# Kernel tuning notes

Measured on AMD Instinct MI355X. Metric: run time of the kernel, lower is better.

## Reference

```python
import jax, jax.numpy as jnp
import numpy as np

B, T, D = 4, 4096, 1024
H, HD = 16, 64
EPS = 1e-6


def setup_inputs() -> dict:
    key = jax.random.key(0)
    ks = jax.random.split(key, 5)
    scale = 1.0 / np.sqrt(D)
    return {
        "x": jax.random.normal(ks[0], (B, T, D), dtype=jnp.float32),
        "Wq": jax.random.normal(ks[1], (D, H * HD), dtype=jnp.float32) * scale,
        "Wk": jax.random.normal(ks[2], (D, H * HD), dtype=jnp.float32) * scale,
        "Wv": jax.random.normal(ks[3], (D, H * HD), dtype=jnp.float32) * scale,
        "Wo": jax.random.normal(ks[4], (H * HD, D), dtype=jnp.float32) * scale,
    }


def _feature_map(x):
    # ELU + 1 feature map (always positive)
    return jax.nn.elu(x) + 1.0


def _causal_linear_attention(q, k, v, eps=EPS):
    # q,k,v: (B,H,T,Dk/Dv) -> scan over T with running state
    Dk = q.shape[-1]
    Dv = v.shape[-1]
    qT = jnp.moveaxis(q, 2, 0)  # (T,B,H,Dk)
    kT = jnp.moveaxis(k, 2, 0)
    vT = jnp.moveaxis(v, 2, 0)

    S0 = jnp.zeros((q.shape[0], q.shape[1], Dk, Dv), dtype=q.dtype)
    z0 = jnp.zeros((q.shape[0], q.shape[1], Dk), dtype=q.dtype)

    def step(carry, qkv_t):
        S, z = carry
        q_t, k_t, v_t = qkv_t
        S = S + jnp.einsum('bhd,bhe->bhde', k_t, v_t)
        z = z + k_t
        num = jnp.einsum('bhd,bhde->bhe', q_t, S)
        den = jnp.einsum('bhd,bhd->bh', q_t, z) + eps
        return (S, z), num / den[..., None]

    _, yT = jax.lax.scan(step, (S0, z0), (qT, kT, vT))  # yT: (T,B,H,Dv)
    return jnp.moveaxis(yT, 0, 2)  # (B,H,T,Dv)


def reference(x, Wq, Wk, Wv, Wo):
    b, t, _ = x.shape

    def proj(W):
        return (x @ W).reshape(b, t, H, HD).transpose(0, 2, 1, 3)  # (B,H,T,HD)

    q = _feature_map(proj(Wq))
    k = _feature_map(proj(Wk))
    v = proj(Wv)
    y = _causal_linear_attention(q, k, v)  # (B,H,T,HD)
    y = y.transpose(0, 2, 1, 3).reshape(b, t, H * HD)
    return y @ Wo
```

## Files before the change

### kernel.cpp

```cpp
#include <hip/hip_runtime.h>


typedef __bf16 bf16;
typedef __bf16 bf16x8 __attribute__((ext_vector_type(8)));
typedef float f32x4 __attribute__((ext_vector_type(4)));

#define EPS 1e-6f

__device__ __forceinline__ void gl_lds16(const void* g, void* l) {
  __builtin_amdgcn_global_load_lds(
      (__attribute__((address_space(1))) void*)g,
      (__attribute__((address_space(3))) void*)l, 16, 0, 0);
}

__device__ __forceinline__ float fmact(float v) {
  return v > 0.f ? v + 1.f : __expf(v);
}

__global__ __launch_bounds__(256) void cvt_bf16(const float* __restrict__ in,
                                                bf16* __restrict__ out, int n8) {
  int i = blockIdx.x * 256 + threadIdx.x;
  if (i >= n8) return;
  size_t base = (size_t)i * 8;
  float4 v0 = *(const float4*)&in[base];
  float4 v1 = *(const float4*)&in[base + 4];
  bf16x8 o;
  o[0] = (bf16)v0.x; o[1] = (bf16)v0.y; o[2] = (bf16)v0.z; o[3] = (bf16)v0.w;
  o[4] = (bf16)v1.x; o[5] = (bf16)v1.y; o[6] = (bf16)v1.z; o[7] = (bf16)v1.w;
  *(bf16x8*)&out[base] = o;
}

__global__ __launch_bounds__(256) void wtrans(const float* __restrict__ W,
                                              bf16* __restrict__ WT) {
  __shared__ float tile[64][65];
  const int k0 = blockIdx.x * 64, n0 = blockIdx.y * 64;
  const int t = threadIdx.x;
  {
    const int r4 = t / 16, c4 = (t % 16) * 4;
#pragma unroll
    for (int rr = 0; rr < 4; ++rr) {
      int r = r4 + rr * 16;
      float4 v = *(const float4*)&W[(size_t)(k0 + r) * 1024 + n0 + c4];
      tile[r][c4] = v.x; tile[r][c4 + 1] = v.y;
      tile[r][c4 + 2] = v.z; tile[r][c4 + 3] = v.w;
    }
  }
  __syncthreads();
  const int nl = t / 4, kb = (t % 4) * 16;
  bf16x8 o0, o1;
#pragma unroll
  for (int j = 0; j < 8; ++j) {
    o0[j] = (bf16)tile[kb + j][nl];
    o1[j] = (bf16)tile[kb + 8 + j][nl];
  }
  *(bf16x8*)&WT[(size_t)(n0 + nl) * 1024 + k0 + kb] = o0;
  *(bf16x8*)&WT[(size_t)(n0 + nl) * 1024 + k0 + kb + 8] = o1;
}

template <int PROJ>
__global__ __launch_bounds__(256) void gemm_bt(const bf16* __restrict__ A,
                                               const bf16* __restrict__ BT,
                                               bf16* __restrict__ Obf,
                                               float* __restrict__ Of, int N) {
  __shared__ alignas(16) bf16 As[128 * 32];
  __shared__ alignas(16) bf16 Bs[128 * 32];
  const int t = threadIdx.x;
  const int m0 = blockIdx.x * 128, n0 = blockIdx.y * 128;
  const int l = t & 63, w = t >> 6;
  const int wm = (w >> 1) * 64, wn = (w & 1) * 64;
  const int lr = l & 15, lg = l >> 4, lk = lg * 8;
  f32x4 acc[4][4] = {};
  const int ar = t >> 2;
  const int ac = (t & 3) * 8;
  bf16* asw = As + w * 512;
  bf16* bsw = Bs + w * 512;
  const bf16* pa0 = A + (size_t)(m0 + ar) * 1024 + ac;
  const bf16* pa1 = A + (size_t)(m0 + ar + 64) * 1024 + ac;
  const bf16* pb0 = BT + (size_t)(n0 + ar) * 1024 + ac;
  const bf16* pb1 = BT + (size_t)(n0 + ar + 64) * 1024 + ac;
  for (int k0 = 0; k0 < 1024; k0 += 32) {
    gl_lds16(pa0 + k0, asw);
    gl_lds16(pa1 + k0, asw + 2048);
    gl_lds16(pb0 + k0, bsw);
    gl_lds16(pb1 + k0, bsw + 2048);
    __syncthreads();
    bf16x8 af[4], bfv[4];
#pragma unroll
    for (int m = 0; m < 4; ++m)
      af[m] = *(const bf16x8*)&As[(wm + m * 16 + lr) * 32 + lk];
#pragma unroll
    for (int n = 0; n < 4; ++n)
      bfv[n] = *(const bf16x8*)&Bs[(wn + n * 16 + lr) * 32 + lk];
#pragma unroll
    for (int m = 0; m < 4; ++m)
#pragma unroll
      for (int n = 0; n < 4; ++n)
        acc[m][n] = __builtin_amdgcn_mfma_f32_16x16x32_bf16(af[m], bfv[n],
                                                            acc[m][n], 0, 0, 0);
    __syncthreads();
  }
  const size_t ldo = (size_t)N;
#pragma unroll
  for (int m = 0; m < 4; ++m)
#pragma unroll
    for (int n = 0; n < 4; ++n)
#pragma unroll
      for (int r = 0; r < 4; ++r) {
        int row = m0 + wm + m * 16 + lg * 4 + r;
        int col = n0 + wn + n * 16 + lr;
        float v = acc[m][n][r];
        if (PROJ) {
          if (col < 2048) v = fmact(v);
          Obf[(size_t)row * ldo + col] = (bf16)v;
        } else {
          Of[(size_t)row * ldo + col] = v;
        }
      }
}

__global__ __launch_bounds__(256) void chunk_ktv(const bf16* __restrict__ QKV,
                                                 float* __restrict__ S_ws,
                                                 float* __restrict__ z_ws) {
  const int blk = blockIdx.x;
  const int bh = blk >> 5, c = blk & 31;
  const int b = bh >> 4, h = bh & 15;
  const size_t rowbase = (size_t)b * 4096 + (size_t)c * 128;
  __shared__ alignas(16) bf16 KT[64 * 136];
  __shared__ alignas(16) bf16 VT[64 * 136];
  const int t = threadIdx.x;
  {
    const int r = t >> 1, c0 = (t & 1) * 32;
    const bf16* kp = QKV + (rowbase + r) * 3072 + 1024 + h * 64 + c0;
    const bf16* vp = QKV + (rowbase + r) * 3072 + 2048 + h * 64 + c0;
    bf16x8 kv[4], vv[4];
#pragma unroll
    for (int q8 = 0; q8 < 4; ++q8) {
      kv[q8] = *(const bf16x8*)&kp[q8 * 8];
      vv[q8] = *(const bf16x8*)&vp[q8 * 8];
    }
#pragma unroll
    for (int q8 = 0; q8 < 4; ++q8)
#pragma unroll
      for (int j = 0; j < 8; ++j) {
        KT[(c0 + q8 * 8 + j) * 136 + r] = kv[q8][j];
        VT[(c0 + q8 * 8 + j) * 136 + r] = vv[q8][j];
      }
  }
  __syncthreads();
  if (t < 64) {
    float z = 0.f;
    for (int tt = 0; tt < 128; ++tt) z += (float)KT[t * 136 + tt];
    z_ws[(size_t)blk * 64 + t] = z;
  }
  const int l = t & 63, w = t >> 6;
  const int lr = l & 15, lg = l >> 4, lk = lg * 8;
  f32x4 acc[4] = {};
#pragma unroll
  for (int ks = 0; ks < 4; ++ks) {
    const int k0 = ks * 32;
    bf16x8 a = *(const bf16x8*)&KT[(w * 16 + lr) * 136 + k0 + lk];
#pragma unroll
    for (int n = 0; n < 4; ++n) {
      bf16x8 bv = *(const bf16x8*)&VT[(n * 16 + lr) * 136 + k0 + lk];
      acc[n] = __builtin_amdgcn_mfma_f32_16x16x32_bf16(a, bv, acc[n], 0, 0, 0);
    }
  }
#pragma unroll
  for (int n = 0; n < 4; ++n)
#pragma unroll
    for (int r = 0; r < 4; ++r) {
      int d = w * 16 + lg * 4 + r;
      int e = n * 16 + lr;
      S_ws[((size_t)blk * 64 + d) * 64 + e] = acc[n][r];
    }
}

__global__ __launch_bounds__(256) void prefix_scan(const float* __restrict__ S_ws,
                                                   const float* __restrict__ z_ws,
                                                   bf16* __restrict__ STp,
                                                   float* __restrict__ zP) {
  const int bh = blockIdx.x;
  const int t = threadIdx.x;
  __shared__ float sbuf[4096];
  float racc[16];
#pragma unroll
  for (int u = 0; u < 16; ++u) racc[u] = 0.f;
  const int e = t >> 2, d0 = (t & 3) * 16;
  float zr = 0.f;
  for (int c = 0; c < 32; ++c) {
    const size_t cb = (size_t)bh * 32 + c;
    bf16x8 o0, o1;
#pragma unroll
    for (int u = 0; u < 8; ++u) {
      o0[u] = (bf16)racc[u];
      o1[u] = (bf16)racc[8 + u];
    }
    *(bf16x8*)&STp[cb * 4096 + e * 64 + d0] = o0;
    *(bf16x8*)&STp[cb * 4096 + e * 64 + d0 + 8] = o1;
    if (t < 64) {
      zP[cb * 64 + t] = zr;
      zr += z_ws[cb * 64 + t];
    }
    const float* Sc = S_ws + cb * 4096;
#pragma unroll
    for (int q4 = 0; q4 < 4; ++q4)
      *(float4*)&sbuf[t * 16 + q4 * 4] = *(const float4*)&Sc[t * 16 + q4 * 4];
    __syncthreads();
#pragma unroll
    for (int u = 0; u < 16; ++u) racc[u] += sbuf[(d0 + u) * 64 + e];
    __syncthreads();
  }
}

__global__ __launch_bounds__(256) void chunk_attn(const bf16* __restrict__ QKV,
                                                  const bf16* __restrict__ STp,
                                                  const float* __restrict__ zP,
                                                  bf16* __restrict__ Y) {
  const int blk = blockIdx.x;
  const int bh = blk >> 5, c = blk & 31;
  const int b = bh >> 4, h = bh & 15;
  const size_t cb = (size_t)bh * 32 + c;
  const size_t rowbase = (size_t)b * 4096 + (size_t)c * 128;
  const bf16* Q = QKV + rowbase * 3072 + h * 64;
  const bf16* K = QKV + rowbase * 3072 + 1024 + h * 64;
  const bf16* V = QKV + rowbase * 3072 + 2048 + h * 64;
  __shared__ alignas(16) bf16 VT[64 * 136];
  __shared__ alignas(16) bf16 P[128 * 136];
  __shared__ float den[128];
  const int t = threadIdx.x;
  {
    const int r = t >> 1, c0 = (t & 1) * 32;
    const bf16* vp = V + (size_t)r * 3072 + c0;
    bf16x8 vv[4];
#pragma unroll
    for (int q8 = 0; q8 < 4; ++q8) vv[q8] = *(const bf16x8*)&vp[q8 * 8];
#pragma unroll
    for (int q8 = 0; q8 < 4; ++q8)
#pragma unroll
      for (int j = 0; j < 8; ++j) VT[(c0 + q8 * 8 + j) * 136 + r] = vv[q8][j];
  }
  const int l = t & 63, w = t >> 6;
  const int lr = l & 15, lg = l >> 4, lk = lg * 8;
  f32x4 acc[2][4] = {};
  f32x4 accs[2][8] = {};
#pragma unroll
  for (int kq = 0; kq < 2; ++kq) {
    const int k0 = kq * 32;
    bf16x8 am[2];
#pragma unroll
    for (int m = 0; m < 2; ++m)
      am[m] = *(const bf16x8*)&Q[(size_t)(w * 32 + m * 16 + lr) * 3072 + k0 + lk];
#pragma unroll
    for (int n = 0; n < 4; ++n) {
      bf16x8 bs = *(const bf16x8*)&STp[cb * 4096 + (size_t)(n * 16 + lr) * 64 + k0 + lk];
#pragma unroll
      for (int m = 0; m < 2; ++m)
        acc[m][n] = __builtin_amdgcn_mfma_f32_16x16x32_bf16(am[m], bs, acc[m][n], 0, 0, 0);
    }
#pragma unroll
    for (int n = 0; n < 8; ++n) {
      bf16x8 bk = *(const bf16x8*)&K[(size_t)(n * 16 + lr) * 3072 + k0 + lk];
#pragma unroll
      for (int m = 0; m < 2; ++m)
        accs[m][n] = __builtin_amdgcn_mfma_f32_16x16x32_bf16(am[m], bk, accs[m][n], 0, 0, 0);
    }
  }
#pragma unroll
  for (int m = 0; m < 2; ++m)
#pragma unroll
    for (int r = 0; r < 4; ++r) {
      const int row_c = w * 32 + m * 16 + lg * 4 + r;
      float s = 0.f;
#pragma unroll
      for (int n = 0; n < 8; ++n) {
        const int col_c = n * 16 + lr;
        float v = accs[m][n][r];
        v = (col_c <= row_c) ? v : 0.f;
        accs[m][n][r] = v;
        s += v;
      }
      s += __shfl_xor(s, 1);
      s += __shfl_xor(s, 2);
      s += __shfl_xor(s, 4);
      s += __shfl_xor(s, 8);
      if (lr == 0) den[row_c] = s;
#pragma unroll
      for (int n = 0; n < 8; ++n)
        P[row_c * 136 + n * 16 + lr] = (bf16)accs[m][n][r];
    }
  __syncthreads();
  if (t < 128) {
    float s = EPS;
    const bf16* qr = Q + (size_t)t * 3072;
    const float* zp = zP + cb * 64;
#pragma unroll
    for (int d8 = 0; d8 < 64; d8 += 8) {
      bf16x8 qv = *(const bf16x8*)&qr[d8];
#pragma unroll
      for (int j = 0; j < 8; ++j) s += (float)qv[j] * zp[d8 + j];
    }
    den[t] += s;
  }
#pragma unroll
  for (int ks = 0; ks < 4; ++ks) {
    const int k0 = ks * 32;
    bf16x8 ap[2];
#pragma unroll
    for (int m = 0; m < 2; ++m)
      ap[m] = *(const bf16x8*)&P[(w * 32 + m * 16 + lr) * 136 + k0 + lk];
#pragma unroll
    for (int n = 0; n < 4; ++n) {
      bf16x8 bv = *(const bf16x8*)&VT[(n * 16 + lr) * 136 + k0 + lk];
#pragma unroll
      for (int m = 0; m < 2; ++m)
        acc[m][n] = __builtin_amdgcn_mfma_f32_16x16x32_bf16(ap[m], bv, acc[m][n], 0, 0, 0);
    }
  }
  __syncthreads();
#pragma unroll
  for (int m = 0; m < 2; ++m)
#pragma unroll
    for (int n = 0; n < 4; ++n)
#pragma unroll
      for (int r = 0; r < 4; ++r) {
        const int row_c = w * 32 + m * 16 + lg * 4 + r;
        const int col = n * 16 + lr;
        float y = acc[m][n][r] / den[row_c];
        Y[(rowbase + row_c) * 1024 + h * 64 + col] = (bf16)y;
      }
}

extern "C" void kernel_launch(void* const* d_in, const int* in_sizes, int n_in,
                              void* d_out, int out_size, void* d_ws, size_t ws_size,
                              hipStream_t stream) {
  (void)in_sizes; (void)n_in; (void)out_size; (void)ws_size;
  const float* x  = (const float*)d_in[0];
  const float* Wq = (const float*)d_in[1];
  const float* Wk = (const float*)d_in[2];
  const float* Wv = (const float*)d_in[3];
  const float* Wo = (const float*)d_in[4];
  char* ws = (char*)d_ws;
  bf16*  XB   = (bf16*)ws;
  bf16*  WT3  = (bf16*)(ws + 33554432);
  bf16*  WOT  = (bf16*)(ws + 39845888);
  bf16*  QKV  = (bf16*)(ws + 41943040);
  float* S_ws = (float*)(ws + 142606336);
  float* z_ws = (float*)(ws + 176160768);
  bf16*  STp  = (bf16*)(ws + 176685056);
  float* zP   = (float*)(ws + 193462272);
  bf16*  Y    = XB;

  cvt_bf16<<<8192, 256, 0, stream>>>(x, XB, 2097152);
  wtrans<<<dim3(16, 16), 256, 0, stream>>>(Wq, WT3);
  wtrans<<<dim3(16, 16), 256, 0, stream>>>(Wk, WT3 + 1048576);
  wtrans<<<dim3(16, 16), 256, 0, stream>>>(Wv, WT3 + 2097152);
  wtrans<<<dim3(16, 16), 256, 0, stream>>>(Wo, WOT);
  gemm_bt<1><<<dim3(128, 24), 256, 0, stream>>>(XB, WT3, QKV, nullptr, 3072);
  chunk_ktv<<<2048, 256, 0, stream>>>(QKV, S_ws, z_ws);
  prefix_scan<<<64, 256, 0, stream>>>(S_ws, z_ws, STp, zP);
  chunk_attn<<<2048, 256, 0, stream>>>(QKV, STp, zP, Y);
  gemm_bt<0><<<dim3(128, 8), 256, 0, stream>>>(Y, WOT, nullptr, (float*)d_out, 1024);
}
```

Baseline: 322.7 us.

## Replace GEMMs with 256x256 double-buffered pipelined kernel and transpose chunk state

Replaces the 128x128 single-buffered GEMM with a 512-thread 256x256-tile kernel. It double-buffers LDS with swizzled layout, interleaves global-to-LDS staging with MFMA phases using manual waitcnt and barriers, raises wave priority around the MFMAs, and remaps blocks for cache locality. The intent is to hide load latency and raise arithmetic intensity in the two dominant projections. Separately, chunk_ktv now writes S transposed so prefix_scan can read it directly with float4 loads, without the LDS transpose and block syncs. The hand-rolled barrier and vmcnt scheme is fragile, and the 128KB LDS per block limits occupancy.

```diff
diff --git a/kernel.cpp b/kernel.cpp
--- a/kernel.cpp
+++ b/kernel.cpp
@@ -6,6 +6,9 @@
 typedef float f32x4 __attribute__((ext_vector_type(4)));
 
 #define EPS 1e-6f
+
+#define BAR() asm volatile("s_barrier" ::: "memory")
+#define VMCNT4() asm volatile("s_waitcnt vmcnt(4)" ::: "memory")
 
 __device__ __forceinline__ void gl_lds16(const void* g, void* l) {
   __builtin_amdgcn_global_load_lds(
@@ -58,50 +61,125 @@
 }
 
 template <int PROJ>
-__global__ __launch_bounds__(256) void gemm_bt(const bf16* __restrict__ A,
-                                               const bf16* __restrict__ BT,
-                                               bf16* __restrict__ Obf,
-                                               float* __restrict__ Of, int N) {
-  __shared__ alignas(16) bf16 As[128 * 32];
-  __shared__ alignas(16) bf16 Bs[128 * 32];
+__global__ __launch_bounds__(512, 2) void gemm4(const bf16* __restrict__ A,
+                                                const bf16* __restrict__ BT,
+                                                bf16* __restrict__ Obf,
+                                                float* __restrict__ Of,
+                                                const int N, const int gy) {
+  extern __shared__ bf16 lds[];
   const int t = threadIdx.x;
-  const int m0 = blockIdx.x * 128, n0 = blockIdx.y * 128;
-  const int l = t & 63, w = t >> 6;
-  const int wm = (w >> 1) * 64, wn = (w & 1) * 64;
-  const int lr = l & 15, lg = l >> 4, lk = lg * 8;
-  f32x4 acc[4][4] = {};
-  const int ar = t >> 2;
-  const int ac = (t & 3) * 8;
-  bf16* asw = As + w * 512;
-  bf16* bsw = Bs + w * 512;
-  const bf16* pa0 = A + (size_t)(m0 + ar) * 1024 + ac;
-  const bf16* pa1 = A + (size_t)(m0 + ar + 64) * 1024 + ac;
-  const bf16* pb0 = BT + (size_t)(n0 + ar) * 1024 + ac;
-  const bf16* pb1 = BT + (size_t)(n0 + ar + 64) * 1024 + ac;
-  for (int k0 = 0; k0 < 1024; k0 += 32) {
-    gl_lds16(pa0 + k0, asw);
-    gl_lds16(pa1 + k0, asw + 2048);
-    gl_lds16(pb0 + k0, bsw);
-    gl_lds16(pb1 + k0, bsw + 2048);
-    __syncthreads();
-    bf16x8 af[4], bfv[4];
+  const int w = t >> 6, l = t & 63;
+  const int nwg = (int)gridDim.x, cpx = nwg >> 3;
+  const int f = ((int)blockIdx.x & 7) * cpx + ((int)blockIdx.x >> 3);
+  const int bx = f / gy, by = f - bx * gy;
+  const int m0 = bx * 256, n0 = by * 256;
+  const int wm = (w >> 2) * 128, wn = (w & 3) * 64;
+  const int lr = l & 15, lg = l >> 4;
+  const int sr = l >> 2;
+  const int sg = (l & 3) ^ ((sr + (sr >> 2)) & 3);
+  const size_t arow0 = (size_t)(m0 + w * 32 + sr);
+  const size_t brow0 = (size_t)(n0 + w * 32 + sr);
+  const bf16* pa0 = A + arow0 * 1024 + sg * 8;
+  const bf16* pa1 = A + (arow0 + 16) * 1024 + sg * 8;
+  const bf16* pb0 = BT + brow0 * 1024 + sg * 8;
+  const bf16* pb1 = BT + (brow0 + 16) * 1024 + sg * 8;
+  const int rswz = (lg ^ ((lr + (lr >> 2)) & 3)) * 8;
+  const int ard = (wm + lr) * 32 + rswz;
+  const int brd = (wn + lr) * 32 + rswz;
+
+  f32x4 acc[8][4] = {};
+
+#define STAGE(nb, ab, ks, kt)                                              \
+  do {                                                                     \
+    const int _ko = (kt) * 64 + (ks) * 32;                                 \
+    bf16* _d = lds + (nb) * 32768 + (ab) * 16384 + (ks) * 8192 + w * 1024; \
+    if (ab) {                                                              \
+      gl_lds16(pb0 + _ko, _d);                                             \
+      gl_lds16(pb1 + _ko, _d + 512);                                       \
+    } else {                                                               \
+      gl_lds16(pa0 + _ko, _d);                                             \
+      gl_lds16(pa1 + _ko, _d + 512);                                       \
+    }                                                                      \
+  } while (0)
+
+  STAGE(0, 0, 0, 0);
+  STAGE(0, 1, 0, 0);
+  STAGE(0, 0, 1, 0);
+  STAGE(0, 1, 1, 0);
+  VMCNT4();
+  BAR();
+
+#pragma unroll 1
+  for (int tt = 0; tt < 16; ++tt) {
+    const int cur = tt & 1, nxt = cur ^ 1;
+    const int kt1 = (tt < 15) ? tt + 1 : 15;
+    const bf16* Ac0 = lds + cur * 32768;
+    const bf16* Ac1 = Ac0 + 8192;
+    const bf16* Bc0 = Ac0 + 16384;
+    const bf16* Bc1 = Bc0 + 8192;
+    bf16x8 av[4], bv[4];
+#pragma unroll
+    for (int m = 0; m < 4; ++m) av[m] = *(const bf16x8*)&Ac0[ard + m * 512];
+#pragma unroll
+    for (int n = 0; n < 4; ++n) bv[n] = *(const bf16x8*)&Bc0[brd + n * 512];
+    STAGE(nxt, 0, 0, kt1);
+    BAR();
+    __builtin_amdgcn_s_setprio(1);
 #pragma unroll
     for (int m = 0; m < 4; ++m)
-      af[m] = *(const bf16x8*)&As[(wm + m * 16 + lr) * 32 + lk];
-#pragma unroll
-    for (int n = 0; n < 4; ++n)
-      bfv[n] = *(const bf16x8*)&Bs[(wn + n * 16 + lr) * 32 + lk];
+#pragma unroll
+      for (int n = 0; n < 4; ++n)
+        acc[m][n] = __builtin_amdgcn_mfma_f32_16x16x32_bf16(av[m], bv[n],
+                                                            acc[m][n], 0, 0, 0);
+    __builtin_amdgcn_s_setprio(0);
+    BAR();
+#pragma unroll
+    for (int m = 0; m < 4; ++m) av[m] = *(const bf16x8*)&Ac0[ard + (m + 4) * 512];
+    STAGE(nxt, 1, 0, kt1);
+    VMCNT4();
+    BAR();
+    __builtin_amdgcn_s_setprio(1);
 #pragma unroll
     for (int m = 0; m < 4; ++m)
 #pragma unroll
       for (int n = 0; n < 4; ++n)
-        acc[m][n] = __builtin_amdgcn_mfma_f32_16x16x32_bf16(af[m], bfv[n],
+        acc[m + 4][n] = __builtin_amdgcn_mfma_f32_16x16x32_bf16(
+            av[m], bv[n], acc[m + 4][n], 0, 0, 0);
+    __builtin_amdgcn_s_setprio(0);
+    BAR();
+#pragma unroll
+    for (int m = 0; m < 4; ++m) av[m] = *(const bf16x8*)&Ac1[ard + m * 512];
+#pragma unroll
+    for (int n = 0; n < 4; ++n) bv[n] = *(const bf16x8*)&Bc1[brd + n * 512];
+    STAGE(nxt, 0, 1, kt1);
+    BAR();
+    __builtin_amdgcn_s_setprio(1);
+#pragma unroll
+    for (int m = 0; m < 4; ++m)
+#pragma unroll
+      for (int n = 0; n < 4; ++n)
+        acc[m][n] = __builtin_amdgcn_mfma_f32_16x16x32_bf16(av[m], bv[n],
                                                             acc[m][n], 0, 0, 0);
-    __syncthreads();
-  }
-  const size_t ldo = (size_t)N;
-#pragma unroll
-  for (int m = 0; m < 4; ++m)
+    __builtin_amdgcn_s_setprio(0);
+    BAR();
+#pragma unroll
+    for (int m = 0; m < 4; ++m) av[m] = *(const bf16x8*)&Ac1[ard + (m + 4) * 512];
+    STAGE(nxt, 1, 1, kt1);
+    VMCNT4();
+    BAR();
+    __builtin_amdgcn_s_setprio(1);
+#pragma unroll
+    for (int m = 0; m < 4; ++m)
+#pragma unroll
+      for (int n = 0; n < 4; ++n)
+        acc[m + 4][n] = __builtin_amdgcn_mfma_f32_16x16x32_bf16(
+            av[m], bv[n], acc[m + 4][n], 0, 0, 0);
+    __builtin_amdgcn_s_setprio(0);
+    BAR();
+  }
+#undef STAGE
+#pragma unroll
+  for (int m = 0; m < 8; ++m)
 #pragma unroll
     for (int n = 0; n < 4; ++n)
 #pragma unroll
@@ -111,9 +189,9 @@
         float v = acc[m][n][r];
         if (PROJ) {
           if (col < 2048) v = fmact(v);
-          Obf[(size_t)row * ldo + col] = (bf16)v;
+          Obf[(size_t)row * N + col] = (bf16)v;
         } else {
-          Of[(size_t)row * ldo + col] = v;
+          Of[(size_t)row * N + col] = v;
         }
       }
 }
@@ -158,20 +236,20 @@
 #pragma unroll
   for (int ks = 0; ks < 4; ++ks) {
     const int k0 = ks * 32;
-    bf16x8 a = *(const bf16x8*)&KT[(w * 16 + lr) * 136 + k0 + lk];
+    bf16x8 a = *(const bf16x8*)&VT[(w * 16 + lr) * 136 + k0 + lk];
 #pragma unroll
     for (int n = 0; n < 4; ++n) {
-      bf16x8 bv = *(const bf16x8*)&VT[(n * 16 + lr) * 136 + k0 + lk];
-      acc[n] = __builtin_amdgcn_mfma_f32_16x16x32_bf16(a, bv, acc[n], 0, 0, 0);
+      bf16x8 bk = *(const bf16x8*)&KT[(n * 16 + lr) * 136 + k0 + lk];
+      acc[n] = __builtin_amdgcn_mfma_f32_16x16x32_bf16(a, bk, acc[n], 0, 0, 0);
     }
   }
 #pragma unroll
   for (int n = 0; n < 4; ++n)
 #pragma unroll
     for (int r = 0; r < 4; ++r) {
-      int d = w * 16 + lg * 4 + r;
-      int e = n * 16 + lr;
-      S_ws[((size_t)blk * 64 + d) * 64 + e] = acc[n][r];
+      int e = w * 16 + lg * 4 + r;
+      int d = n * 16 + lr;
+      S_ws[((size_t)blk * 64 + e) * 64 + d] = acc[n][r];
     }
 }
 
@@ -181,11 +259,10 @@
                                                    float* __restrict__ zP) {
   const int bh = blockIdx.x;
   const int t = threadIdx.x;
-  __shared__ float sbuf[4096];
+  const int e = t >> 2, d0 = (t & 3) * 16;
   float racc[16];
 #pragma unroll
   for (int u = 0; u < 16; ++u) racc[u] = 0.f;
-  const int e = t >> 2, d0 = (t & 3) * 16;
   float zr = 0.f;
   for (int c = 0; c < 32; ++c) {
     const size_t cb = (size_t)bh * 32 + c;
@@ -201,14 +278,14 @@
       zP[cb * 64 + t] = zr;
       zr += z_ws[cb * 64 + t];
     }
-    const float* Sc = S_ws + cb * 4096;
-#pragma unroll
-    for (int q4 = 0; q4 < 4; ++q4)
-      *(float4*)&sbuf[t * 16 + q4 * 4] = *(const float4*)&Sc[t * 16 + q4 * 4];
-    __syncthreads();
-#pragma unroll
-    for (int u = 0; u < 16; ++u) racc[u] += sbuf[(d0 + u) * 64 + e];
-    __syncthreads();
+#pragma unroll
+    for (int q = 0; q < 4; ++q) {
+      float4 v = *(const float4*)&S_ws[cb * 4096 + e * 64 + d0 + q * 4];
+      racc[q * 4 + 0] += v.x;
+      racc[q * 4 + 1] += v.y;
+      racc[q * 4 + 2] += v.z;
+      racc[q * 4 + 3] += v.w;
+    }
   }
 }
 
@@ -350,14 +427,22 @@
   float* zP   = (float*)(ws + 193462272);
   bf16*  Y    = XB;
 
+  {
+    auto k1 = gemm4<1>; auto k0 = gemm4<0>;
+    (void)hipFuncSetAttribute((const void*)k1,
+        hipFuncAttributeMaxDynamicSharedMemorySize, 131072);
+    (void)hipFuncSetAttribute((const void*)k0,
+        hipFuncAttributeMaxDynamicSharedMemorySize, 131072);
+  }
+
   cvt_bf16<<<8192, 256, 0, stream>>>(x, XB, 2097152);
   wtrans<<<dim3(16, 16), 256, 0, stream>>>(Wq, WT3);
   wtrans<<<dim3(16, 16), 256, 0, stream>>>(Wk, WT3 + 1048576);
   wtrans<<<dim3(16, 16), 256, 0, stream>>>(Wv, WT3 + 2097152);
   wtrans<<<dim3(16, 16), 256, 0, stream>>>(Wo, WOT);
-  gemm_bt<1><<<dim3(128, 24), 256, 0, stream>>>(XB, WT3, QKV, nullptr, 3072);
+  gemm4<1><<<768, 512, 131072, stream>>>(XB, WT3, QKV, nullptr, 3072, 12);
   chunk_ktv<<<2048, 256, 0, stream>>>(QKV, S_ws, z_ws);
   prefix_scan<<<64, 256, 0, stream>>>(S_ws, z_ws, STp, zP);
   chunk_attn<<<2048, 256, 0, stream>>>(QKV, STp, zP, Y);
-  gemm_bt<0><<<dim3(128, 8), 256, 0, stream>>>(Y, WOT, nullptr, (float*)d_out, 1024);
-}
+  gemm4<0><<<256, 512, 131072, stream>>>(Y, WOT, nullptr, (float*)d_out, 1024, 4);
+}
```

Measured after the change: 287.3 us. 11.0% less time.
